# Kernel tuning notes

Hardware: AMD Instinct MI355X
Metric: run time of the kernel (lower is better)

Reference implementation:

```python
import jax, jax.numpy as jnp
import numpy as np

B, S, F = 4, 2048, 512
H, DK, DV, FILT = 8, 64, 64, 512

def setup_inputs() -> dict:
    key = jax.random.key(0)
    ks = jax.random.split(key, 11)
    sc_in = 1.0 / np.sqrt(F)
    sc_o = 1.0 / np.sqrt(H * DV)
    return {
        "x_q": jax.random.normal(ks[0], (B, S, F), jnp.float32),
        "x_k": jax.random.normal(ks[1], (B, S, F), jnp.float32),
        "x_v": jax.random.normal(ks[2], (B, S, F), jnp.float32),
        "Wq": jax.random.normal(ks[3], (H, F, DK), jnp.float32) * sc_in,
        "bq": jax.random.normal(ks[4], (H, DK), jnp.float32) * 0.01,
        "Wk": jax.random.normal(ks[5], (H, F, DK), jnp.float32) * sc_in,
        "bk": jax.random.normal(ks[6], (H, DK), jnp.float32) * 0.01,
        "Wv": jax.random.normal(ks[7], (H, F, DV), jnp.float32) * sc_in,
        "bv": jax.random.normal(ks[8], (H, DV), jnp.float32) * 0.01,
        "Wo": jax.random.normal(ks[9], (H * DV, FILT), jnp.float32) * sc_o,
        "bo": jax.random.normal(ks[10], (FILT,), jnp.float32) * 0.01,
    }

def reference(x_q, x_k, x_v, Wq, bq, Wk, bk, Wv, bv, Wo, bo):
    d_k = Wq.shape[-1]
    # per-head Dense projections, batched over heads: [B,H,S,dk/dv]
    q = jnp.einsum("bsf,hfk->bhsk", x_q, Wq) + bq[:, None, :]
    k = jnp.einsum("bsf,hfk->bhsk", x_k, Wk) + bk[:, None, :]
    v = jnp.einsum("bsf,hfv->bhsv", x_v, Wv) + bv[:, None, :]
    # scaled dot-product attention (scale by 1/sqrt(d_k) as in map_fn)
    scores = jnp.einsum("bhsk,bhtk->bhst", q, k) / jnp.sqrt(jnp.asarray(d_k, q.dtype))
    attn = jax.nn.softmax(scores, axis=-1)
    out = jnp.einsum("bhst,bhtv->bhsv", attn, v)
    # concat heads along feature dim -> [B,S,H*DV], then output linear
    bsz, h, s, dv = out.shape
    concat = out.transpose(0, 2, 1, 3).reshape(bsz, s, h * dv)
    return concat @ Wo + bo
```

## Files before the change

### kernel.cpp

```cpp
#include <hip/hip_runtime.h>

#define B_    4
#define S_    2048
#define H_    8
#define M_    (B_ * S_)

typedef __bf16    bf16_t;
typedef _Float16  f16_t;
typedef __bf16   bf16x8 __attribute__((ext_vector_type(8)));
typedef __bf16   bf16x4 __attribute__((ext_vector_type(4)));
typedef _Float16 f16x8  __attribute__((ext_vector_type(8)));
typedef float    f32x16 __attribute__((ext_vector_type(16)));

union B8 { uint4 u; bf16x8 v; bf16_t e[8]; };
union B4 { uint2 u; bf16x4 v; bf16_t e[4]; };
union H8 { uint4 u; f16x8  v; f16_t  e[8]; };
union H4 { uint2 u; f16_t  e[4]; };

#define QSCALE 0.1803368801111204f

__global__ __launch_bounds__(256) void convert_w(
    const float* __restrict__ w0, const float* __restrict__ w1,
    const float* __restrict__ w2, bf16_t* __restrict__ t0,
    bf16_t* __restrict__ t1, bf16_t* __restrict__ t2)
{
    __shared__ float T[64][65];
    const float* W  = blockIdx.z == 0 ? w0 : blockIdx.z == 1 ? w1 : w2;
    bf16_t*      Wt = blockIdx.z == 0 ? t0 : blockIdx.z == 1 ? t1 : t2;
    const int h  = blockIdx.y;
    const int k0 = blockIdx.x * 64;
    const int tid = threadIdx.x;
    const int row = tid & 63, q4 = tid >> 6;

    const float* Wh = W + (size_t)h * 512 * 64;
    #pragma unroll
    for (int i = 0; i < 4; ++i) {
        int fq = q4 * 4 + i;
        float4 v = *(const float4*)(Wh + (size_t)(k0 + row) * 64 + fq * 4);
        T[row][fq * 4 + 0] = v.x; T[row][fq * 4 + 1] = v.y;
        T[row][fq * 4 + 2] = v.z; T[row][fq * 4 + 3] = v.w;
    }
    __syncthreads();
    bf16_t* Wth = Wt + (size_t)h * 64 * 512;
    #pragma unroll
    for (int i = 0; i < 4; ++i) {
        int kq = q4 * 4 + i;
        B4 o;
        #pragma unroll
        for (int j = 0; j < 4; ++j) o.e[j] = (bf16_t)T[kq * 4 + j][row];
        *(uint2*)(Wth + (size_t)row * 512 + k0 + kq * 4) = o.u;
    }
}

__global__ __launch_bounds__(256) void convert_wo(
    const float* __restrict__ Wo, f16_t* __restrict__ Wot)
{
    __shared__ float T[64][65];
    const int k0 = blockIdx.x * 64;
    const int n0 = blockIdx.y * 64;
    const int tid = threadIdx.x;
    const int row = tid & 63, q4 = tid >> 6;

    #pragma unroll
    for (int i = 0; i < 4; ++i) {
        int fq = q4 * 4 + i;
        float4 v = *(const float4*)(Wo + (size_t)(k0 + row) * 512 + n0 + fq * 4);
        T[row][fq * 4 + 0] = v.x; T[row][fq * 4 + 1] = v.y;
        T[row][fq * 4 + 2] = v.z; T[row][fq * 4 + 3] = v.w;
    }
    __syncthreads();
    #pragma unroll
    for (int i = 0; i < 4; ++i) {
        int kq = q4 * 4 + i;
        H4 o;
        #pragma unroll
        for (int j = 0; j < 4; ++j) o.e[j] = (f16_t)T[kq * 4 + j][row];
        *(uint2*)(Wot + (size_t)(n0 + row) * 512 + k0 + kq * 4) = o.u;
    }
}

__global__ __launch_bounds__(256) void proj_tiled(
    const float* __restrict__ xq, const float* __restrict__ xk,
    const float* __restrict__ xv,
    const bf16_t* __restrict__ Wtq, const bf16_t* __restrict__ Wtk,
    const bf16_t* __restrict__ Wtv,
    const float* __restrict__ bq, const float* __restrict__ bk,
    const float* __restrict__ bv,
    bf16_t* __restrict__ Qb, bf16_t* __restrict__ Kb, bf16_t* __restrict__ Vt)
{
    __shared__ bf16_t As[128 * 72];
    __shared__ bf16_t Bs[128 * 72];

    const int z = blockIdx.z;
    const float*  X    = z == 0 ? xq  : z == 1 ? xk  : xv;
    const bf16_t* Wt   = z == 0 ? Wtq : z == 1 ? Wtk : Wtv;
    const float*  bias = z == 0 ? bq  : z == 1 ? bk  : bv;

    const int tid  = threadIdx.x;
    const int wave = tid >> 6, lane = tid & 63;
    const int l31  = lane & 31, half = lane >> 5;
    const int m0   = blockIdx.x * 128;
    const int n0   = blockIdx.y * 128;
    const int mw   = (wave & 1) * 64;
    const int nw   = (wave >> 1) * 64;

    const int sr = tid >> 1;
    const int sc = (tid & 1) * 32;

    float4 ra0[4], ra1[4];
    uint4  rb[4];
    {
        const float*  ap = X  + (size_t)(m0 + sr) * 512 + sc;
        const bf16_t* bp = Wt + (size_t)(n0 + sr) * 512 + sc;
        #pragma unroll
        for (int i = 0; i < 4; ++i) {
            ra0[i] = *(const float4*)(ap + i * 8);
            ra1[i] = *(const float4*)(ap + i * 8 + 4);
            rb[i]  = *(const uint4*)(bp + i * 8);
        }
    }

    f32x16 acc[2][2];
    #pragma unroll
    for (int mt = 0; mt < 2; ++mt)
        #pragma unroll
        for (int nt = 0; nt < 2; ++nt)
            #pragma unroll
            for (int i = 0; i < 16; ++i) acc[mt][nt][i] = 0.0f;

    for (int k0 = 0; k0 < 512; k0 += 64) {
        __syncthreads();
        #pragma unroll
        for (int i = 0; i < 4; ++i) {
            B8 w;
            w.e[0] = (bf16_t)ra0[i].x; w.e[1] = (bf16_t)ra0[i].y;
            w.e[2] = (bf16_t)ra0[i].z; w.e[3] = (bf16_t)ra0[i].w;
            w.e[4] = (bf16_t)ra1[i].x; w.e[5] = (bf16_t)ra1[i].y;
            w.e[6] = (bf16_t)ra1[i].z; w.e[7] = (bf16_t)ra1[i].w;
            *(uint4*)&As[sr * 72 + sc + i * 8] = w.u;
            *(uint4*)&Bs[sr * 72 + sc + i * 8] = rb[i];
        }
        if (k0 + 64 < 512) {
            const float*  ap = X  + (size_t)(m0 + sr) * 512 + k0 + 64 + sc;
            const bf16_t* bp = Wt + (size_t)(n0 + sr) * 512 + k0 + 64 + sc;
            #pragma unroll
            for (int i = 0; i < 4; ++i) {
                ra0[i] = *(const float4*)(ap + i * 8);
                ra1[i] = *(const float4*)(ap + i * 8 + 4);
                rb[i]  = *(const uint4*)(bp + i * 8);
            }
        }
        __syncthreads();

        #pragma unroll
        for (int kc = 0; kc < 4; ++kc) {
            B8 a0, a1, b0, b1;
            a0.u = *(const uint4*)&As[(mw + l31)      * 72 + kc * 16 + half * 8];
            a1.u = *(const uint4*)&As[(mw + 32 + l31) * 72 + kc * 16 + half * 8];
            b0.u = *(const uint4*)&Bs[(nw + l31)      * 72 + kc * 16 + half * 8];
            b1.u = *(const uint4*)&Bs[(nw + 32 + l31) * 72 + kc * 16 + half * 8];
            acc[0][0] = __builtin_amdgcn_mfma_f32_32x32x16_bf16(a0.v, b0.v, acc[0][0], 0, 0, 0);
            acc[0][1] = __builtin_amdgcn_mfma_f32_32x32x16_bf16(a0.v, b1.v, acc[0][1], 0, 0, 0);
            acc[1][0] = __builtin_amdgcn_mfma_f32_32x32x16_bf16(a1.v, b0.v, acc[1][0], 0, 0, 0);
            acc[1][1] = __builtin_amdgcn_mfma_f32_32x32x16_bf16(a1.v, b1.v, acc[1][1], 0, 0, 0);
        }
    }

    if (z <= 1) {
        const float sc_ = (z == 0) ? QSCALE : 1.0f;
        bf16_t* Out = (z == 0) ? Qb : Kb;
        #pragma unroll
        for (int mt = 0; mt < 2; ++mt)
            #pragma unroll
            for (int nt = 0; nt < 2; ++nt) {
                int n = n0 + nw + nt * 32 + l31;
                float bv_ = bias[n];
                #pragma unroll
                for (int r = 0; r < 16; ++r) {
                    int m = m0 + mw + mt * 32 + (r & 3) + 8 * (r >> 2) + 4 * half;
                    Out[(size_t)m * 512 + n] = (bf16_t)((acc[mt][nt][r] + bv_) * sc_);
                }
            }
    } else {
        const int b  = m0 >> 11;
        const int sb = (m0 & 2047);
        #pragma unroll
        for (int mt = 0; mt < 2; ++mt)
            #pragma unroll
            for (int nt = 0; nt < 2; ++nt) {
                int n = n0 + nw + nt * 32 + l31;
                float bv_ = bias[n];
                int h = n >> 6, d = n & 63;
                bf16_t* base = Vt + ((size_t)(b * 8 + h) * 64 + d) * 2048 + sb + mw + mt * 32;
                #pragma unroll
                for (int g = 0; g < 4; ++g) {
                    B4 p;
                    #pragma unroll
                    for (int j = 0; j < 4; ++j) p.e[j] = (bf16_t)(acc[mt][nt][g * 4 + j] + bv_);
                    *(uint2*)(base + 8 * g + 4 * half) = p.u;
                }
            }
    }
}

__global__ __launch_bounds__(512) void attn_mfma(
    const bf16_t* __restrict__ Q, const bf16_t* __restrict__ K,
    const bf16_t* __restrict__ Vt, f16_t* __restrict__ O)
{
    __shared__ char smraw[36864];
    bf16_t* KsBuf = (bf16_t*)smraw;
    bf16_t* VsBuf = KsBuf + 2 * 64 * 72;

    const int bh  = blockIdx.y;
    const int b   = bh >> 3, h = bh & 7;
    const int q0  = blockIdx.x * 128;
    const int tid = threadIdx.x;
    const int wave = tid >> 6, lane = tid & 63;
    const int l31 = lane & 31, half = lane >> 5;
    const int qsub = wave & 3, ksplit = wave >> 2;

    bf16x8 qf[4];
    {
        const bf16_t* qp = Q + ((size_t)(b * S_ + q0 + qsub * 32 + l31)) * 512 + h * 64 + half * 8;
        #pragma unroll
        for (int ks = 0; ks < 4; ++ks) {
            B8 t; t.u = *(const uint4*)(qp + ks * 16);
            qf[ks] = t.v;
        }
    }

    f32x16 o0, o1;
    #pragma unroll
    for (int i = 0; i < 16; ++i) { o0[i] = 0.0f; o1[i] = 0.0f; }
    float l_i = 0.0f;

    const bf16_t* Kbase = K + ((size_t)b * S_) * 512 + h * 64;
    const bf16_t* Vbase = Vt + ((size_t)bh * 64) * 2048;

    const int sbuf = tid >> 8;
    const int p    = tid & 255;
    const int kr = p >> 3, kc8 = p & 7;
    const int vd = p >> 2, vj = p & 3;
    const int kqmap[4] = {0, 2, 1, 3};
    const int vkq = kqmap[vj];
    bf16_t* KsS = KsBuf + sbuf * (64 * 72);
    bf16_t* VsS = VsBuf + sbuf * (64 * 72);
    const bf16_t* KsC = KsBuf + ksplit * (64 * 72);
    const bf16_t* VsC = VsBuf + ksplit * (64 * 72);

    for (int t0 = 0; t0 < 1024; t0 += 64) {
        const int tb = sbuf * 1024 + t0;
        __syncthreads();
        #pragma unroll
        for (int l = 0; l < 2; ++l) {
            int row = kr + 32 * l;
            *(uint4*)&KsS[row * 72 + kc8 * 8] =
                *(const uint4*)(Kbase + (size_t)(tb + row) * 512 + kc8 * 8);
        }
        #pragma unroll
        for (int g = 0; g < 4; ++g) {
            *(uint2*)&VsS[vd * 72 + g * 16 + vj * 4] =
                *(const uint2*)(Vbase + (size_t)vd * 2048 + tb + g * 16 + vkq * 4);
        }
        __syncthreads();

        f32x16 s0, s1;
        #pragma unroll
        for (int i = 0; i < 16; ++i) { s0[i] = 0.0f; s1[i] = 0.0f; }
        #pragma unroll
        for (int ks = 0; ks < 4; ++ks) {
            B8 k0, k1;
            k0.u = *(const uint4*)(&KsC[l31 * 72 + ks * 16 + half * 8]);
            k1.u = *(const uint4*)(&KsC[(32 + l31) * 72 + ks * 16 + half * 8]);
            s0 = __builtin_amdgcn_mfma_f32_32x32x16_bf16(k0.v, qf[ks], s0, 0, 0, 0);
            s1 = __builtin_amdgcn_mfma_f32_32x32x16_bf16(k1.v, qf[ks], s1, 0, 0, 0);
        }

        float ls = 0.0f;
        #pragma unroll
        for (int r = 0; r < 16; ++r) {
            s0[r] = __builtin_amdgcn_exp2f(s0[r]); ls += s0[r];
            s1[r] = __builtin_amdgcn_exp2f(s1[r]); ls += s1[r];
        }
        l_i += ls;

        B8 pf[4];
        #pragma unroll
        for (int j = 0; j < 8; ++j) {
            pf[0].e[j] = (bf16_t)s0[j];
            pf[1].e[j] = (bf16_t)s0[8 + j];
            pf[2].e[j] = (bf16_t)s1[j];
            pf[3].e[j] = (bf16_t)s1[8 + j];
        }

        #pragma unroll
        for (int c = 0; c < 4; ++c) {
            B8 va, vb;
            va.u = *(const uint4*)(&VsC[l31 * 72 + c * 16 + half * 8]);
            vb.u = *(const uint4*)(&VsC[(32 + l31) * 72 + c * 16 + half * 8]);
            o0 = __builtin_amdgcn_mfma_f32_32x32x16_bf16(va.v, pf[c].v, o0, 0, 0, 0);
            o1 = __builtin_amdgcn_mfma_f32_32x32x16_bf16(vb.v, pf[c].v, o1, 0, 0, 0);
        }
    }

    l_i += __shfl_xor(l_i, 32);
    __syncthreads();
    float* co = (float*)smraw;
    float* cl = co + 4 * 32 * 68;
    if (ksplit == 1) {
        float* reg = co + qsub * (32 * 68);
        #pragma unroll
        for (int r = 0; r < 16; ++r) {
            reg[r * 68 + lane]        = o0[r];
            reg[(16 + r) * 68 + lane] = o1[r];
        }
        cl[qsub * 64 + lane] = l_i;
    }
    __syncthreads();
    if (ksplit == 0) {
        float* reg = co + qsub * (32 * 68);
        float inv = 1.0f / (l_i + cl[qsub * 64 + lane]);
        f16_t* Ob = O + ((size_t)(b * S_ + q0 + qsub * 32 + l31)) * 512 + h * 64;
        #pragma unroll
        for (int g = 0; g < 4; ++g) {
            H4 a, c;
            #pragma unroll
            for (int j = 0; j < 4; ++j) {
                int r = g * 4 + j;
                a.e[j] = (f16_t)((o0[r] + reg[r * 68 + lane]) * inv);
                c.e[j] = (f16_t)((o1[r] + reg[(16 + r) * 68 + lane]) * inv);
            }
            int d = 8 * g + 4 * half;
            *(uint2*)(Ob + d)      = a.u;
            *(uint2*)(Ob + 32 + d) = c.u;
        }
    }
}

__global__ __launch_bounds__(256) void gemm_out_tiled(
    const f16_t* __restrict__ A, const f16_t* __restrict__ Wot,
    const float* __restrict__ bias, float* __restrict__ C)
{
    __shared__ f16_t As[64 * 72];
    __shared__ f16_t Bs[64 * 72];

    const int tid  = threadIdx.x;
    const int wave = tid >> 6, lane = tid & 63;
    const int l31  = lane & 31, half = lane >> 5;
    const int m0   = blockIdx.x * 64;
    const int n0   = blockIdx.y * 64;
    const int mw   = (wave & 1) * 32;
    const int nw   = (wave >> 1) * 32;

    const int sr  = tid >> 2;
    const int so  = (tid & 3) * 16;

    uint4 pA0, pA1, pB0, pB1;
    {
        const f16_t* ap = A   + (size_t)(m0 + sr) * 512 + so;
        const f16_t* bp = Wot + (size_t)(n0 + sr) * 512 + so;
        pA0 = *(const uint4*)(ap); pA1 = *(const uint4*)(ap + 8);
        pB0 = *(const uint4*)(bp); pB1 = *(const uint4*)(bp + 8);
    }

    f32x16 acc;
    #pragma unroll
    for (int i = 0; i < 16; ++i) acc[i] = 0.0f;

    for (int k0 = 0; k0 < 512; k0 += 64) {
        __syncthreads();
        *(uint4*)&As[sr * 72 + so]     = pA0;
        *(uint4*)&As[sr * 72 + so + 8] = pA1;
        *(uint4*)&Bs[sr * 72 + so]     = pB0;
        *(uint4*)&Bs[sr * 72 + so + 8] = pB1;
        if (k0 + 64 < 512) {
            const f16_t* ap = A   + (size_t)(m0 + sr) * 512 + k0 + 64 + so;
            const f16_t* bp = Wot + (size_t)(n0 + sr) * 512 + k0 + 64 + so;
            pA0 = *(const uint4*)(ap); pA1 = *(const uint4*)(ap + 8);
            pB0 = *(const uint4*)(bp); pB1 = *(const uint4*)(bp + 8);
        }
        __syncthreads();

        #pragma unroll
        for (int kc = 0; kc < 4; ++kc) {
            H8 a, b;
            a.u = *(const uint4*)&As[(mw + l31) * 72 + kc * 16 + half * 8];
            b.u = *(const uint4*)&Bs[(nw + l31) * 72 + kc * 16 + half * 8];
            acc = __builtin_amdgcn_mfma_f32_32x32x16_f16(a.v, b.v, acc, 0, 0, 0);
        }
    }

    const int n = n0 + nw + l31;
    const float bias0 = bias[n];
    #pragma unroll
    for (int r = 0; r < 16; ++r) {
        int m = m0 + mw + (r & 3) + 8 * (r >> 2) + 4 * half;
        C[(size_t)m * 512 + n] = acc[r] + bias0;
    }
}

extern "C" void kernel_launch(void* const* d_in, const int* in_sizes, int n_in,
                              void* d_out, int out_size, void* d_ws, size_t ws_size,
                              hipStream_t stream)
{
    const float* x_q = (const float*)d_in[0];
    const float* x_k = (const float*)d_in[1];
    const float* x_v = (const float*)d_in[2];
    const float* Wq  = (const float*)d_in[3];
    const float* bq  = (const float*)d_in[4];
    const float* Wk  = (const float*)d_in[5];
    const float* bk  = (const float*)d_in[6];
    const float* Wv  = (const float*)d_in[7];
    const float* bv  = (const float*)d_in[8];
    const float* Wo  = (const float*)d_in[9];
    const float* bo  = (const float*)d_in[10];
    float* out = (float*)d_out;

    char* W = (char*)d_ws;
    bf16_t* Wtq = (bf16_t*)W;
    bf16_t* Wtk = Wtq + (size_t)8 * 64 * 512;
    bf16_t* Wtv = Wtk + (size_t)8 * 64 * 512;
    f16_t*  Wot = (f16_t*)(Wtv + (size_t)8 * 64 * 512);
    bf16_t* Qb  = (bf16_t*)(Wot + (size_t)512 * 512);
    bf16_t* Kb  = Qb + (size_t)M_ * 512;
    bf16_t* Vt  = Kb + (size_t)M_ * 512;
    f16_t*  AO  = (f16_t*)(Vt + (size_t)M_ * 512);

    convert_w<<<dim3(8, 8, 3), 256, 0, stream>>>(Wq, Wk, Wv, Wtq, Wtk, Wtv);
    convert_wo<<<dim3(8, 8), 256, 0, stream>>>(Wo, Wot);

    proj_tiled<<<dim3(64, 4, 3), 256, 0, stream>>>(
        x_q, x_k, x_v, Wtq, Wtk, Wtv, bq, bk, bv, Qb, Kb, Vt);

    attn_mfma<<<dim3(S_ / 128, B_ * H_), 512, 0, stream>>>(Qb, Kb, Vt, AO);

    gemm_out_tiled<<<dim3(128, 8), 256, 0, stream>>>(AO, Wot, bo, out);
}
```

Before: 222.5 us.

## Merge weight conversion kernels and halve projection and attention block tiles

The two weight-conversion kernels become one launch with a fourth z-slice that handles Wo. The projection GEMM tile shrinks from 128x128 to 64x128 (one MFMA row tile per wave), and attention blocks drop from 512 threads and 128 queries to 256 threads and 64 queries, with the K/V staging loops reworked to match. Together these double the block count for both kernels and cut one launch, aiming at better CU occupancy and less launch overhead. In exchange, each K/V tile is reused by fewer queries, so more global and LDS traffic is spent per query.

```diff
diff --git a/kernel.cpp b/kernel.cpp
--- a/kernel.cpp
+++ b/kernel.cpp
@@ -19,63 +19,58 @@
 
 #define QSCALE 0.1803368801111204f
 
-__global__ __launch_bounds__(256) void convert_w(
+__global__ __launch_bounds__(256) void convert_weights(
     const float* __restrict__ w0, const float* __restrict__ w1,
-    const float* __restrict__ w2, bf16_t* __restrict__ t0,
-    bf16_t* __restrict__ t1, bf16_t* __restrict__ t2)
+    const float* __restrict__ w2, const float* __restrict__ wo,
+    bf16_t* __restrict__ t0, bf16_t* __restrict__ t1,
+    bf16_t* __restrict__ t2, f16_t* __restrict__ wot)
 {
     __shared__ float T[64][65];
-    const float* W  = blockIdx.z == 0 ? w0 : blockIdx.z == 1 ? w1 : w2;
-    bf16_t*      Wt = blockIdx.z == 0 ? t0 : blockIdx.z == 1 ? t1 : t2;
-    const int h  = blockIdx.y;
-    const int k0 = blockIdx.x * 64;
+    const int z   = blockIdx.z;
+    const int k0  = blockIdx.x * 64;
     const int tid = threadIdx.x;
     const int row = tid & 63, q4 = tid >> 6;
 
-    const float* Wh = W + (size_t)h * 512 * 64;
-    #pragma unroll
-    for (int i = 0; i < 4; ++i) {
-        int fq = q4 * 4 + i;
-        float4 v = *(const float4*)(Wh + (size_t)(k0 + row) * 64 + fq * 4);
-        T[row][fq * 4 + 0] = v.x; T[row][fq * 4 + 1] = v.y;
-        T[row][fq * 4 + 2] = v.z; T[row][fq * 4 + 3] = v.w;
-    }
-    __syncthreads();
-    bf16_t* Wth = Wt + (size_t)h * 64 * 512;
-    #pragma unroll
-    for (int i = 0; i < 4; ++i) {
-        int kq = q4 * 4 + i;
-        B4 o;
-        #pragma unroll
-        for (int j = 0; j < 4; ++j) o.e[j] = (bf16_t)T[kq * 4 + j][row];
-        *(uint2*)(Wth + (size_t)row * 512 + k0 + kq * 4) = o.u;
-    }
-}
-
-__global__ __launch_bounds__(256) void convert_wo(
-    const float* __restrict__ Wo, f16_t* __restrict__ Wot)
-{
-    __shared__ float T[64][65];
-    const int k0 = blockIdx.x * 64;
-    const int n0 = blockIdx.y * 64;
-    const int tid = threadIdx.x;
-    const int row = tid & 63, q4 = tid >> 6;
-
-    #pragma unroll
-    for (int i = 0; i < 4; ++i) {
-        int fq = q4 * 4 + i;
-        float4 v = *(const float4*)(Wo + (size_t)(k0 + row) * 512 + n0 + fq * 4);
-        T[row][fq * 4 + 0] = v.x; T[row][fq * 4 + 1] = v.y;
-        T[row][fq * 4 + 2] = v.z; T[row][fq * 4 + 3] = v.w;
-    }
-    __syncthreads();
-    #pragma unroll
-    for (int i = 0; i < 4; ++i) {
-        int kq = q4 * 4 + i;
-        H4 o;
-        #pragma unroll
-        for (int j = 0; j < 4; ++j) o.e[j] = (f16_t)T[kq * 4 + j][row];
-        *(uint2*)(Wot + (size_t)(n0 + row) * 512 + k0 + kq * 4) = o.u;
+    if (z < 3) {
+        const float* W  = z == 0 ? w0 : z == 1 ? w1 : w2;
+        bf16_t*      Wt = z == 0 ? t0 : z == 1 ? t1 : t2;
+        const int h = blockIdx.y;
+        const float* Wh = W + (size_t)h * 512 * 64;
+        #pragma unroll
+        for (int i = 0; i < 4; ++i) {
+            int fq = q4 * 4 + i;
+            float4 v = *(const float4*)(Wh + (size_t)(k0 + row) * 64 + fq * 4);
+            T[row][fq * 4 + 0] = v.x; T[row][fq * 4 + 1] = v.y;
+            T[row][fq * 4 + 2] = v.z; T[row][fq * 4 + 3] = v.w;
+        }
+        __syncthreads();
+        bf16_t* Wth = Wt + (size_t)h * 64 * 512;
+        #pragma unroll
+        for (int i = 0; i < 4; ++i) {
+            int kq = q4 * 4 + i;
+            B4 o;
+            #pragma unroll
+            for (int j = 0; j < 4; ++j) o.e[j] = (bf16_t)T[kq * 4 + j][row];
+            *(uint2*)(Wth + (size_t)row * 512 + k0 + kq * 4) = o.u;
+        }
+    } else {
+        const int n0 = blockIdx.y * 64;
+        #pragma unroll
+        for (int i = 0; i < 4; ++i) {
+            int fq = q4 * 4 + i;
+            float4 v = *(const float4*)(wo + (size_t)(k0 + row) * 512 + n0 + fq * 4);
+            T[row][fq * 4 + 0] = v.x; T[row][fq * 4 + 1] = v.y;
+            T[row][fq * 4 + 2] = v.z; T[row][fq * 4 + 3] = v.w;
+        }
+        __syncthreads();
+        #pragma unroll
+        for (int i = 0; i < 4; ++i) {
+            int kq = q4 * 4 + i;
+            H4 o;
+            #pragma unroll
+            for (int j = 0; j < 4; ++j) o.e[j] = (f16_t)T[kq * 4 + j][row];
+            *(uint2*)(wot + (size_t)(n0 + row) * 512 + k0 + kq * 4) = o.u;
+        }
     }
 }
 
@@ -88,7 +83,7 @@
     const float* __restrict__ bv,
     bf16_t* __restrict__ Qb, bf16_t* __restrict__ Kb, bf16_t* __restrict__ Vt)
 {
-    __shared__ bf16_t As[128 * 72];
+    __shared__ bf16_t As[64 * 72];
     __shared__ bf16_t Bs[128 * 72];
 
     const int z = blockIdx.z;
@@ -99,70 +94,67 @@
     const int tid  = threadIdx.x;
     const int wave = tid >> 6, lane = tid & 63;
     const int l31  = lane & 31, half = lane >> 5;
-    const int m0   = blockIdx.x * 128;
+    const int m0   = blockIdx.x * 64;
     const int n0   = blockIdx.y * 128;
-    const int mw   = (wave & 1) * 64;
+    const int mw   = (wave & 1) * 32;
     const int nw   = (wave >> 1) * 64;
 
-    const int sr = tid >> 1;
-    const int sc = (tid & 1) * 32;
-
-    float4 ra0[4], ra1[4];
+    const int sra = tid >> 2, sca = (tid & 3) * 16;
+    const int srb = tid >> 1, scb = (tid & 1) * 32;
+
+    float4 ra[4];
     uint4  rb[4];
     {
-        const float*  ap = X  + (size_t)(m0 + sr) * 512 + sc;
-        const bf16_t* bp = Wt + (size_t)(n0 + sr) * 512 + sc;
+        const float*  ap = X  + (size_t)(m0 + sra) * 512 + sca;
+        const bf16_t* bp = Wt + (size_t)(n0 + srb) * 512 + scb;
         #pragma unroll
         for (int i = 0; i < 4; ++i) {
-            ra0[i] = *(const float4*)(ap + i * 8);
-            ra1[i] = *(const float4*)(ap + i * 8 + 4);
-            rb[i]  = *(const uint4*)(bp + i * 8);
-        }
-    }
-
-    f32x16 acc[2][2];
+            ra[i] = *(const float4*)(ap + i * 4);
+            rb[i] = *(const uint4*)(bp + i * 8);
+        }
+    }
+
+    f32x16 acc0, acc1;
     #pragma unroll
-    for (int mt = 0; mt < 2; ++mt)
-        #pragma unroll
-        for (int nt = 0; nt < 2; ++nt)
-            #pragma unroll
-            for (int i = 0; i < 16; ++i) acc[mt][nt][i] = 0.0f;
+    for (int i = 0; i < 16; ++i) { acc0[i] = 0.0f; acc1[i] = 0.0f; }
 
     for (int k0 = 0; k0 < 512; k0 += 64) {
         __syncthreads();
-        #pragma unroll
-        for (int i = 0; i < 4; ++i) {
-            B8 w;
-            w.e[0] = (bf16_t)ra0[i].x; w.e[1] = (bf16_t)ra0[i].y;
-            w.e[2] = (bf16_t)ra0[i].z; w.e[3] = (bf16_t)ra0[i].w;
-            w.e[4] = (bf16_t)ra1[i].x; w.e[5] = (bf16_t)ra1[i].y;
-            w.e[6] = (bf16_t)ra1[i].z; w.e[7] = (bf16_t)ra1[i].w;
-            *(uint4*)&As[sr * 72 + sc + i * 8] = w.u;
-            *(uint4*)&Bs[sr * 72 + sc + i * 8] = rb[i];
+        {
+            B8 w0, w1;
+            w0.e[0] = (bf16_t)ra[0].x; w0.e[1] = (bf16_t)ra[0].y;
+            w0.e[2] = (bf16_t)ra[0].z; w0.e[3] = (bf16_t)ra[0].w;
+            w0.e[4] = (bf16_t)ra[1].x; w0.e[5] = (bf16_t)ra[1].y;
+            w0.e[6] = (bf16_t)ra[1].z; w0.e[7] = (bf16_t)ra[1].w;
+            w1.e[0] = (bf16_t)ra[2].x; w1.e[1] = (bf16_t)ra[2].y;
+            w1.e[2] = (bf16_t)ra[2].z; w1.e[3] = (bf16_t)ra[2].w;
+            w1.e[4] = (bf16_t)ra[3].x; w1.e[5] = (bf16_t)ra[3].y;
+            w1.e[6] = (bf16_t)ra[3].z; w1.e[7] = (bf16_t)ra[3].w;
+            *(uint4*)&As[sra * 72 + sca]     = w0.u;
+            *(uint4*)&As[sra * 72 + sca + 8] = w1.u;
+            #pragma unroll
+            for (int i = 0; i < 4; ++i)
+                *(uint4*)&Bs[srb * 72 + scb + i * 8] = rb[i];
         }
         if (k0 + 64 < 512) {
-            const float*  ap = X  + (size_t)(m0 + sr) * 512 + k0 + 64 + sc;
-            const bf16_t* bp = Wt + (size_t)(n0 + sr) * 512 + k0 + 64 + sc;
+            const float*  ap = X  + (size_t)(m0 + sra) * 512 + k0 + 64 + sca;
+            const bf16_t* bp = Wt + (size_t)(n0 + srb) * 512 + k0 + 64 + scb;
             #pragma unroll
             for (int i = 0; i < 4; ++i) {
-                ra0[i] = *(const float4*)(ap + i * 8);
-                ra1[i] = *(const float4*)(ap + i * 8 + 4);
-                rb[i]  = *(const uint4*)(bp + i * 8);
+                ra[i] = *(const float4*)(ap + i * 4);
+                rb[i] = *(const uint4*)(bp + i * 8);
             }
         }
         __syncthreads();
 
         #pragma unroll
         for (int kc = 0; kc < 4; ++kc) {
-            B8 a0, a1, b0, b1;
-            a0.u = *(const uint4*)&As[(mw + l31)      * 72 + kc * 16 + half * 8];
-            a1.u = *(const uint4*)&As[(mw + 32 + l31) * 72 + kc * 16 + half * 8];
+            B8 a, b0, b1;
+            a.u  = *(const uint4*)&As[(mw + l31)      * 72 + kc * 16 + half * 8];
             b0.u = *(const uint4*)&Bs[(nw + l31)      * 72 + kc * 16 + half * 8];
             b1.u = *(const uint4*)&Bs[(nw + 32 + l31) * 72 + kc * 16 + half * 8];
-            acc[0][0] = __builtin_amdgcn_mfma_f32_32x32x16_bf16(a0.v, b0.v, acc[0][0], 0, 0, 0);
-            acc[0][1] = __builtin_amdgcn_mfma_f32_32x32x16_bf16(a0.v, b1.v, acc[0][1], 0, 0, 0);
-            acc[1][0] = __builtin_amdgcn_mfma_f32_32x32x16_bf16(a1.v, b0.v, acc[1][0], 0, 0, 0);
-            acc[1][1] = __builtin_amdgcn_mfma_f32_32x32x16_bf16(a1.v, b1.v, acc[1][1], 0, 0, 0);
+            acc0 = __builtin_amdgcn_mfma_f32_32x32x16_bf16(a.v, b0.v, acc0, 0, 0, 0);
+            acc1 = __builtin_amdgcn_mfma_f32_32x32x16_bf16(a.v, b1.v, acc1, 0, 0, 0);
         }
     }
 
@@ -170,40 +162,38 @@
         const float sc_ = (z == 0) ? QSCALE : 1.0f;
         bf16_t* Out = (z == 0) ? Qb : Kb;
         #pragma unroll
-        for (int mt = 0; mt < 2; ++mt)
-            #pragma unroll
-            for (int nt = 0; nt < 2; ++nt) {
-                int n = n0 + nw + nt * 32 + l31;
-                float bv_ = bias[n];
-                #pragma unroll
-                for (int r = 0; r < 16; ++r) {
-                    int m = m0 + mw + mt * 32 + (r & 3) + 8 * (r >> 2) + 4 * half;
-                    Out[(size_t)m * 512 + n] = (bf16_t)((acc[mt][nt][r] + bv_) * sc_);
-                }
+        for (int nt = 0; nt < 2; ++nt) {
+            int n = n0 + nw + nt * 32 + l31;
+            float bv_ = bias[n];
+            const f32x16& ac = nt ? acc1 : acc0;
+            #pragma unroll
+            for (int r = 0; r < 16; ++r) {
+                int m = m0 + mw + (r & 3) + 8 * (r >> 2) + 4 * half;
+                Out[(size_t)m * 512 + n] = (bf16_t)((ac[r] + bv_) * sc_);
             }
+        }
     } else {
         const int b  = m0 >> 11;
-        const int sb = (m0 & 2047);
-        #pragma unroll
-        for (int mt = 0; mt < 2; ++mt)
-            #pragma unroll
-            for (int nt = 0; nt < 2; ++nt) {
-                int n = n0 + nw + nt * 32 + l31;
-                float bv_ = bias[n];
-                int h = n >> 6, d = n & 63;
-                bf16_t* base = Vt + ((size_t)(b * 8 + h) * 64 + d) * 2048 + sb + mw + mt * 32;
+        const int sb = (m0 & 2047) + mw;
+        #pragma unroll
+        for (int nt = 0; nt < 2; ++nt) {
+            int n = n0 + nw + nt * 32 + l31;
+            float bv_ = bias[n];
+            int h = n >> 6, d = n & 63;
+            const f32x16& ac = nt ? acc1 : acc0;
+            bf16_t* base = Vt + ((size_t)(b * 8 + h) * 64 + d) * 2048 + sb;
+            #pragma unroll
+            for (int g = 0; g < 4; ++g) {
+                B4 p;
                 #pragma unroll
-                for (int g = 0; g < 4; ++g) {
-                    B4 p;
-                    #pragma unroll
-                    for (int j = 0; j < 4; ++j) p.e[j] = (bf16_t)(acc[mt][nt][g * 4 + j] + bv_);
-                    *(uint2*)(base + 8 * g + 4 * half) = p.u;
-                }
+                for (int j = 0; j < 4; ++j) p.e[j] = (bf16_t)(ac[g * 4 + j] + bv_);
+                *(uint2*)(base + 8 * g + 4 * half) = p.u;
             }
+        }
     }
 }
 
-__global__ __launch_bounds__(512) void attn_mfma(
+__global__ __launch_bounds__(256) void attn_mfma(
     const bf16_t* __restrict__ Q, const bf16_t* __restrict__ K,
     const bf16_t* __restrict__ Vt, f16_t* __restrict__ O)
 {
@@ -213,11 +203,11 @@
 
     const int bh  = blockIdx.y;
     const int b   = bh >> 3, h = bh & 7;
-    const int q0  = blockIdx.x * 128;
+    const int q0  = blockIdx.x * 64;
     const int tid = threadIdx.x;
     const int wave = tid >> 6, lane = tid & 63;
     const int l31 = lane & 31, half = lane >> 5;
-    const int qsub = wave & 3, ksplit = wave >> 2;
+    const int qsub = wave & 1, ksplit = wave >> 1;
 
     bf16x8 qf[4];
     {
@@ -237,11 +227,10 @@
     const bf16_t* Kbase = K + ((size_t)b * S_) * 512 + h * 64;
     const bf16_t* Vbase = Vt + ((size_t)bh * 64) * 2048;
 
-    const int sbuf = tid >> 8;
-    const int p    = tid & 255;
-    const int kr = p >> 3, kc8 = p & 7;
-    const int vd = p >> 2, vj = p & 3;
+    const int sbuf = tid >> 7;
+    const int p    = tid & 127;
     const int kqmap[4] = {0, 2, 1, 3};
+    const int vj  = p & 3;
     const int vkq = kqmap[vj];
     bf16_t* KsS = KsBuf + sbuf * (64 * 72);
     bf16_t* VsS = VsBuf + sbuf * (64 * 72);
@@ -252,15 +241,19 @@
         const int tb = sbuf * 1024 + t0;
         __syncthreads();
         #pragma unroll
+        for (int l = 0; l < 4; ++l) {
+            int idx = p + l * 128;
+            int row = idx >> 3, c8 = idx & 7;
+            *(uint4*)&KsS[row * 72 + c8 * 8] =
+                *(const uint4*)(Kbase + (size_t)(tb + row) * 512 + c8 * 8);
+        }
+        #pragma unroll
         for (int l = 0; l < 2; ++l) {
-            int row = kr + 32 * l;
-            *(uint4*)&KsS[row * 72 + kc8 * 8] =
-                *(const uint4*)(Kbase + (size_t)(tb + row) * 512 + kc8 * 8);
-        }
-        #pragma unroll
-        for (int g = 0; g < 4; ++g) {
-            *(uint2*)&VsS[vd * 72 + g * 16 + vj * 4] =
-                *(const uint2*)(Vbase + (size_t)vd * 2048 + tb + g * 16 + vkq * 4);
+            int vd = (p >> 2) + 32 * l;
+            #pragma unroll
+            for (int g = 0; g < 4; ++g)
+                *(uint2*)&VsS[vd * 72 + g * 16 + vj * 4] =
+                    *(const uint2*)(Vbase + (size_t)vd * 2048 + tb + g * 16 + vkq * 4);
         }
         __syncthreads();
 
@@ -306,7 +299,7 @@
     l_i += __shfl_xor(l_i, 32);
     __syncthreads();
     float* co = (float*)smraw;
-    float* cl = co + 4 * 32 * 68;
+    float* cl = co + 2 * 32 * 68;
     if (ksplit == 1) {
         float* reg = co + qsub * (32 * 68);
         #pragma unroll
@@ -426,13 +419,13 @@
     bf16_t* Vt  = Kb + (size_t)M_ * 512;
     f16_t*  AO  = (f16_t*)(Vt + (size_t)M_ * 512);
 
-    convert_w<<<dim3(8, 8, 3), 256, 0, stream>>>(Wq, Wk, Wv, Wtq, Wtk, Wtv);
-    convert_wo<<<dim3(8, 8), 256, 0, stream>>>(Wo, Wot);
-
-    proj_tiled<<<dim3(64, 4, 3), 256, 0, stream>>>(
+    convert_weights<<<dim3(8, 8, 4), 256, 0, stream>>>(
+        Wq, Wk, Wv, Wo, Wtq, Wtk, Wtv, Wot);
+
+    proj_tiled<<<dim3(128, 4, 3), 256, 0, stream>>>(
         x_q, x_k, x_v, Wtq, Wtk, Wtv, bq, bk, bv, Qb, Kb, Vt);
 
-    attn_mfma<<<dim3(S_ / 128, B_ * H_), 512, 0, stream>>>(Qb, Kb, Vt, AO);
+    attn_mfma<<<dim3(S_ / 64, B_ * H_), 256, 0, stream>>>(Qb, Kb, Vt, AO);
 
     gemm_out_tiled<<<dim3(128, 8), 256, 0, stream>>>(AO, Wot, bo, out);
 }
```

New measurement: 294.5 us. 32.4% more time.

## Register-prefetch K/V tiles in attention and merge weight conversion kernels

Applied to the files above, without the earlier changes.

The attention kernel now loads the next K/V tile from global memory into registers while the current tile is being computed, then writes it to LDS at the start of the next iteration. This hides global load latency behind MFMA work. The projection and output GEMMs move their barrier ahead of the next prefetch so the global loads are issued after the LDS stores complete. The two weight-conversion kernels are merged into one launch to save launch overhead. The cost is extra registers in attention, which may lower occupancy.

```diff
diff --git a/kernel.cpp b/kernel.cpp
--- a/kernel.cpp
+++ b/kernel.cpp
@@ -19,63 +19,58 @@
 
 #define QSCALE 0.1803368801111204f
 
-__global__ __launch_bounds__(256) void convert_w(
+__global__ __launch_bounds__(256) void convert_weights(
     const float* __restrict__ w0, const float* __restrict__ w1,
-    const float* __restrict__ w2, bf16_t* __restrict__ t0,
-    bf16_t* __restrict__ t1, bf16_t* __restrict__ t2)
+    const float* __restrict__ w2, const float* __restrict__ wo,
+    bf16_t* __restrict__ t0, bf16_t* __restrict__ t1,
+    bf16_t* __restrict__ t2, f16_t* __restrict__ wot)
 {
     __shared__ float T[64][65];
-    const float* W  = blockIdx.z == 0 ? w0 : blockIdx.z == 1 ? w1 : w2;
-    bf16_t*      Wt = blockIdx.z == 0 ? t0 : blockIdx.z == 1 ? t1 : t2;
-    const int h  = blockIdx.y;
-    const int k0 = blockIdx.x * 64;
+    const int z   = blockIdx.z;
+    const int k0  = blockIdx.x * 64;
     const int tid = threadIdx.x;
     const int row = tid & 63, q4 = tid >> 6;
 
-    const float* Wh = W + (size_t)h * 512 * 64;
-    #pragma unroll
-    for (int i = 0; i < 4; ++i) {
-        int fq = q4 * 4 + i;
-        float4 v = *(const float4*)(Wh + (size_t)(k0 + row) * 64 + fq * 4);
-        T[row][fq * 4 + 0] = v.x; T[row][fq * 4 + 1] = v.y;
-        T[row][fq * 4 + 2] = v.z; T[row][fq * 4 + 3] = v.w;
-    }
-    __syncthreads();
-    bf16_t* Wth = Wt + (size_t)h * 64 * 512;
-    #pragma unroll
-    for (int i = 0; i < 4; ++i) {
-        int kq = q4 * 4 + i;
-        B4 o;
-        #pragma unroll
-        for (int j = 0; j < 4; ++j) o.e[j] = (bf16_t)T[kq * 4 + j][row];
-        *(uint2*)(Wth + (size_t)row * 512 + k0 + kq * 4) = o.u;
-    }
-}
-
-__global__ __launch_bounds__(256) void convert_wo(
-    const float* __restrict__ Wo, f16_t* __restrict__ Wot)
-{
-    __shared__ float T[64][65];
-    const int k0 = blockIdx.x * 64;
-    const int n0 = blockIdx.y * 64;
-    const int tid = threadIdx.x;
-    const int row = tid & 63, q4 = tid >> 6;
-
-    #pragma unroll
-    for (int i = 0; i < 4; ++i) {
-        int fq = q4 * 4 + i;
-        float4 v = *(const float4*)(Wo + (size_t)(k0 + row) * 512 + n0 + fq * 4);
-        T[row][fq * 4 + 0] = v.x; T[row][fq * 4 + 1] = v.y;
-        T[row][fq * 4 + 2] = v.z; T[row][fq * 4 + 3] = v.w;
-    }
-    __syncthreads();
-    #pragma unroll
-    for (int i = 0; i < 4; ++i) {
-        int kq = q4 * 4 + i;
-        H4 o;
-        #pragma unroll
-        for (int j = 0; j < 4; ++j) o.e[j] = (f16_t)T[kq * 4 + j][row];
-        *(uint2*)(Wot + (size_t)(n0 + row) * 512 + k0 + kq * 4) = o.u;
+    if (z < 3) {
+        const float* W  = z == 0 ? w0 : z == 1 ? w1 : w2;
+        bf16_t*      Wt = z == 0 ? t0 : z == 1 ? t1 : t2;
+        const int h = blockIdx.y;
+        const float* Wh = W + (size_t)h * 512 * 64;
+        #pragma unroll
+        for (int i = 0; i < 4; ++i) {
+            int fq = q4 * 4 + i;
+            float4 v = *(const float4*)(Wh + (size_t)(k0 + row) * 64 + fq * 4);
+            T[row][fq * 4 + 0] = v.x; T[row][fq * 4 + 1] = v.y;
+            T[row][fq * 4 + 2] = v.z; T[row][fq * 4 + 3] = v.w;
+        }
+        __syncthreads();
+        bf16_t* Wth = Wt + (size_t)h * 64 * 512;
+        #pragma unroll
+        for (int i = 0; i < 4; ++i) {
+            int kq = q4 * 4 + i;
+            B4 o;
+            #pragma unroll
+            for (int j = 0; j < 4; ++j) o.e[j] = (bf16_t)T[kq * 4 + j][row];
+            *(uint2*)(Wth + (size_t)row * 512 + k0 + kq * 4) = o.u;
+        }
+    } else {
+        const int n0 = blockIdx.y * 64;
+        #pragma unroll
+        for (int i = 0; i < 4; ++i) {
+            int fq = q4 * 4 + i;
+            float4 v = *(const float4*)(wo + (size_t)(k0 + row) * 512 + n0 + fq * 4);
+            T[row][fq * 4 + 0] = v.x; T[row][fq * 4 + 1] = v.y;
+            T[row][fq * 4 + 2] = v.z; T[row][fq * 4 + 3] = v.w;
+        }
+        __syncthreads();
+        #pragma unroll
+        for (int i = 0; i < 4; ++i) {
+            int kq = q4 * 4 + i;
+            H4 o;
+            #pragma unroll
+            for (int j = 0; j < 4; ++j) o.e[j] = (f16_t)T[kq * 4 + j][row];
+            *(uint2*)(wot + (size_t)(n0 + row) * 512 + k0 + kq * 4) = o.u;
+        }
     }
 }
 
@@ -140,6 +135,7 @@
             *(uint4*)&As[sr * 72 + sc + i * 8] = w.u;
             *(uint4*)&Bs[sr * 72 + sc + i * 8] = rb[i];
         }
+        __syncthreads();
         if (k0 + 64 < 512) {
             const float*  ap = X  + (size_t)(m0 + sr) * 512 + k0 + 64 + sc;
             const bf16_t* bp = Wt + (size_t)(n0 + sr) * 512 + k0 + 64 + sc;
@@ -150,7 +146,6 @@
                 rb[i]  = *(const uint4*)(bp + i * 8);
             }
         }
-        __syncthreads();
 
         #pragma unroll
         for (int kc = 0; kc < 4; ++kc) {
@@ -248,21 +243,34 @@
     const bf16_t* KsC = KsBuf + ksplit * (64 * 72);
     const bf16_t* VsC = VsBuf + ksplit * (64 * 72);
 
+    uint4 kreg0, kreg1;
+    uint2 vreg[4];
+    {
+        const int tb = sbuf * 1024;
+        kreg0 = *(const uint4*)(Kbase + (size_t)(tb + kr) * 512 + kc8 * 8);
+        kreg1 = *(const uint4*)(Kbase + (size_t)(tb + kr + 32) * 512 + kc8 * 8);
+        #pragma unroll
+        for (int g = 0; g < 4; ++g)
+            vreg[g] = *(const uint2*)(Vbase + (size_t)vd * 2048 + tb + g * 16 + vkq * 4);
+    }
+
     for (int t0 = 0; t0 < 1024; t0 += 64) {
-        const int tb = sbuf * 1024 + t0;
-        __syncthreads();
-        #pragma unroll
-        for (int l = 0; l < 2; ++l) {
-            int row = kr + 32 * l;
-            *(uint4*)&KsS[row * 72 + kc8 * 8] =
-                *(const uint4*)(Kbase + (size_t)(tb + row) * 512 + kc8 * 8);
-        }
-        #pragma unroll
-        for (int g = 0; g < 4; ++g) {
-            *(uint2*)&VsS[vd * 72 + g * 16 + vj * 4] =
-                *(const uint2*)(Vbase + (size_t)vd * 2048 + tb + g * 16 + vkq * 4);
-        }
-        __syncthreads();
+        __syncthreads();
+        *(uint4*)&KsS[kr * 72 + kc8 * 8]        = kreg0;
+        *(uint4*)&KsS[(kr + 32) * 72 + kc8 * 8] = kreg1;
+        #pragma unroll
+        for (int g = 0; g < 4; ++g)
+            *(uint2*)&VsS[vd * 72 + g * 16 + vj * 4] = vreg[g];
+        __syncthreads();
+
+        if (t0 + 64 < 1024) {
+            const int tb = sbuf * 1024 + t0 + 64;
+            kreg0 = *(const uint4*)(Kbase + (size_t)(tb + kr) * 512 + kc8 * 8);
+            kreg1 = *(const uint4*)(Kbase + (size_t)(tb + kr + 32) * 512 + kc8 * 8);
+            #pragma unroll
+            for (int g = 0; g < 4; ++g)
+                vreg[g] = *(const uint2*)(Vbase + (size_t)vd * 2048 + tb + g * 16 + vkq * 4);
+        }
 
         f32x16 s0, s1;
         #pragma unroll
@@ -373,13 +381,13 @@
         *(uint4*)&As[sr * 72 + so + 8] = pA1;
         *(uint4*)&Bs[sr * 72 + so]     = pB0;
         *(uint4*)&Bs[sr * 72 + so + 8] = pB1;
+        __syncthreads();
         if (k0 + 64 < 512) {
             const f16_t* ap = A   + (size_t)(m0 + sr) * 512 + k0 + 64 + so;
             const f16_t* bp = Wot + (size_t)(n0 + sr) * 512 + k0 + 64 + so;
             pA0 = *(const uint4*)(ap); pA1 = *(const uint4*)(ap + 8);
             pB0 = *(const uint4*)(bp); pB1 = *(const uint4*)(bp + 8);
         }
-        __syncthreads();
 
         #pragma unroll
         for (int kc = 0; kc < 4; ++kc) {
@@ -426,8 +434,8 @@
     bf16_t* Vt  = Kb + (size_t)M_ * 512;
     f16_t*  AO  = (f16_t*)(Vt + (size_t)M_ * 512);
 
-    convert_w<<<dim3(8, 8, 3), 256, 0, stream>>>(Wq, Wk, Wv, Wtq, Wtk, Wtv);
-    convert_wo<<<dim3(8, 8), 256, 0, stream>>>(Wo, Wot);
+    convert_weights<<<dim3(8, 8, 4), 256, 0, stream>>>(
+        Wq, Wk, Wv, Wo, Wtq, Wtk, Wtv, Wot);
 
     proj_tiled<<<dim3(64, 4, 3), 256, 0, stream>>>(
         x_q, x_k, x_v, Wtq, Wtk, Wtv, bq, bk, bv, Qb, Kb, Vt);
```

After: 214.5 us. 3.6% less time.
